# Optimization experiments

Measured on AMD Instinct MI355X. Metric: run time of the kernel, lower is better.

## Reference

```python
import jax, jax.numpy as jnp
import numpy as np

B, C, L, H = 4, 128, 4096, 4
GROUPS, EPS = 32, 1e-5


def group_norm(x, gamma, beta):
    # x: [B, C, L]; normalize per (batch, group) over (C//G, L)
    b, c, l = x.shape
    xg = x.reshape(b, GROUPS, c // GROUPS, l)
    mu = jnp.mean(xg, axis=(2, 3), keepdims=True)
    var = jnp.var(xg, axis=(2, 3), keepdims=True)
    xn = ((xg - mu) * jax.lax.rsqrt(var + EPS)).reshape(b, c, l)
    return xn * gamma[None, :, None] + beta[None, :, None]


def setup_inputs() -> dict:
    key = jax.random.key(0)
    k1, k2, k3 = jax.random.split(key, 3)
    return {
        "x": jax.random.normal(k1, (B, C, L), dtype=jnp.float32),
        "w_qkv": jax.random.normal(k2, (3 * C, C), dtype=jnp.float32) * 0.02,
        "w_proj": jax.random.normal(k3, (C, C), dtype=jnp.float32) * 0.02,
        "b_proj": jnp.zeros((C,), dtype=jnp.float32),
        "gn_gamma": jnp.ones((C,), dtype=jnp.float32),
        "gn_beta": jnp.zeros((C,), dtype=jnp.float32),
    }


def reference(x, w_qkv, w_proj, b_proj, gn_gamma, gn_beta):
    b, c, l = x.shape
    hd = c // H
    h = group_norm(x, gn_gamma, gn_beta)
    # 1x1 conv == channel matmul: [B, 3C, L]
    qkv = jnp.einsum('oc,bcl->bol', w_qkv, h)
    # torch reshape(B*H, 3C/H, L).chunk(3, dim=1): per-head contiguous slices
    qkv = qkv.reshape(b, H, 3 * hd, l)
    q, k, v = qkv[:, :, :hd], qkv[:, :, hd:2 * hd], qkv[:, :, 2 * hd:]
    scale = 1.0 / np.sqrt(np.sqrt(hd)).astype(np.float32)
    attn = jnp.einsum('bhct,bhcs->bhts', q * scale, k * scale)
    attn = jax.nn.softmax(attn, axis=-1)
    o = jnp.einsum('bhts,bhcs->bhct', attn, v).reshape(b, c, l)
    o = jnp.einsum('oc,bcl->bol', w_proj, o) + b_proj[None, :, None]
    return o + x
```

## Files before the change

### kernel.cpp

```cpp
#include <hip/hip_runtime.h>
#include <hip/hip_bf16.h>
#include <cstdint>
#include <cstddef>


#define B_ 4
#define C_ 128
#define L_ 4096
#define H_ 4
#define HD_ 32
#define NG_ 32
#define CPG_ 4
#define EPS_ 1e-5f
#define QKSCALE_ 0.5050097650430367f

typedef __attribute__((ext_vector_type(8))) short bf16x8;
typedef __attribute__((ext_vector_type(8))) unsigned short u16x8;
typedef __attribute__((ext_vector_type(4))) float f32x4;
typedef __attribute__((ext_vector_type(2))) _Float16 f16x2;
typedef __attribute__((ext_vector_type(4))) _Float16 f16x4;

#if __has_builtin(__builtin_amdgcn_exp2f)
#define EXP2F(x) __builtin_amdgcn_exp2f(x)
#else
#define EXP2F(x) exp2f(x)
#endif

#if __has_builtin(__builtin_amdgcn_mfma_f32_16x16x16f16)
#define MFMA_PV(a, b, c) __builtin_amdgcn_mfma_f32_16x16x16f16((a), (b), (c), 0, 0, 0)
#else
#define MFMA_PV(a, b, c) __builtin_amdgcn_mfma_f32_16x16x16f16((a), (b), (c), 0, 0, 0)
#endif

__device__ __forceinline__ float bu2f(unsigned short u) {
  return __builtin_bit_cast(float, (unsigned int)(((unsigned int)u) << 16));
}
__device__ __forceinline__ unsigned short f2bu(float f) {
  unsigned int u = __builtin_bit_cast(unsigned int, f);
  unsigned int r = (u + 0x7fffu + ((u >> 16) & 1u)) >> 16;
  return (unsigned short)r;
}
__device__ __forceinline__ float4 u42f4(ushort4 u) {
  return make_float4(bu2f(u.x), bu2f(u.y), bu2f(u.z), bu2f(u.w));
}
__device__ __forceinline__ unsigned int pkbf(float a, float b) {
  return (unsigned int)f2bu(a) | ((unsigned int)f2bu(b) << 16);
}
__device__ __forceinline__ f16x2 pkhf2(float a, float b) {
#if __has_builtin(__builtin_amdgcn_cvt_pkrtz)
  return __builtin_bit_cast(f16x2, __builtin_amdgcn_cvt_pkrtz(a, b));
#else
  f16x2 r;
  r[0] = (_Float16)a;
  r[1] = (_Float16)b;
  return r;
#endif
}
__device__ __forceinline__ unsigned int pkhf(float a, float b) {
  return __builtin_bit_cast(unsigned int, pkhf2(a, b));
}

__device__ __forceinline__ bool detect_fast(const ushort* x) {
  __shared__ int flag_s;
  int t = threadIdx.x;
  if (t < 64) {
    int e = (x[t] >> 7) & 0xFF;
    unsigned long long m = __ballot((e < 64) || (e > 192));
    if (t == 0) flag_s = (__popcll(m) > 4) ? 1 : 0;
  }
  __syncthreads();
  return flag_s != 0;
}

__device__ __forceinline__ float4 ldx4(const void* x, size_t idx, bool f32) {
  if (f32) return *((const float4*)x + (idx >> 2));
  ushort4 u = *((const ushort4*)x + (idx >> 2));
  return u42f4(u);
}

__global__ __launch_bounds__(256) void gn_stats(const void* __restrict__ x,
                                                const void* __restrict__ wq,
                                                const void* __restrict__ wp,
                                                const void* __restrict__ bp,
                                                const void* __restrict__ gm,
                                                const void* __restrict__ bt,
                                                ushort* __restrict__ wq_b,
                                                ushort* __restrict__ wp_b,
                                                float* __restrict__ bp_f,
                                                float2* __restrict__ gn_ab) {
  bool f32 = detect_fast((const ushort*)x);
  int blk = blockIdx.x;
  int t = threadIdx.x;

  if (blk >= 128) {
    int i0 = ((blk - 128) * 256 + t) * 8;
#pragma unroll
    for (int k = 0; k < 8; ++k) {
      int i = i0 + k;
      if (i >= 65664) break;
      if (i < 49152) {
        wq_b[i] = f32 ? f2bu(((const float*)wq)[i]) : ((const ushort*)wq)[i];
      } else if (i < 65536) {
        int off = i - 49152;
        wp_b[off] = f32 ? f2bu(((const float*)wp)[off]) : ((const ushort*)wp)[off];
      } else {
        int off = i - 65536;
        bp_f[off] = f32 ? ((const float*)bp)[off] : bu2f(((const ushort*)bp)[off]);
      }
    }
    return;
  }

  int b = blk >> 5, g = blk & 31;
  size_t base = ((size_t)b * C_ + (size_t)g * CPG_) * L_;

  float s = 0.f, ss = 0.f;
#pragma unroll
  for (int i = 0; i < 16; ++i) {
    size_t e = base + i * 1024 + t * 4;
    float4 f = ldx4(x, e, f32);
    s += f.x + f.y + f.z + f.w;
    ss += f.x * f.x + f.y * f.y + f.z * f.z + f.w * f.w;
  }
#pragma unroll
  for (int m = 32; m >= 1; m >>= 1) {
    s += __shfl_xor(s, m, 64);
    ss += __shfl_xor(ss, m, 64);
  }
  __shared__ float red[4][2];
  int wv = t >> 6;
  if ((t & 63) == 0) { red[wv][0] = s; red[wv][1] = ss; }
  __syncthreads();
  float ts = red[0][0] + red[1][0] + red[2][0] + red[3][0];
  float tss = red[0][1] + red[1][1] + red[2][1] + red[3][1];
  float mu = ts * (1.0f / 16384.0f);
  float var = tss * (1.0f / 16384.0f) - mu * mu;
  float rs = rsqrtf(var + EPS_);

  if (t < CPG_) {
    int gi = g * CPG_ + t;
    float ga = f32 ? ((const float*)gm)[gi] : bu2f(((const ushort*)gm)[gi]);
    float be = f32 ? ((const float*)bt)[gi] : bu2f(((const ushort*)bt)[gi]);
    gn_ab[b * C_ + gi] = make_float2(ga * rs, be - mu * ga * rs);
  }
}

__global__ __launch_bounds__(256) void qkv_kernel(const ushort* __restrict__ wq_b,
                                                  const void* __restrict__ x,
                                                  const float2* __restrict__ gn_ab,
                                                  ushort* __restrict__ Qt,
                                                  ushort* __restrict__ Kt,
                                                  ushort* __restrict__ Vb) {
  bool f32 = detect_fast((const ushort*)x);
  __shared__ alignas(16) ushort Hs[64][136];
  __shared__ alignas(16) float Ls[64][69];

  int lx = blockIdx.x, oz = blockIdx.y, b = blockIdx.z;
  int t = threadIdx.x;
  int w = t >> 6, lane = t & 63, l16 = lane & 15, q = lane >> 4, q8 = q * 8;

  {
    int u = t & 63, lh = (t >> 6) * 16;
    int c0 = 2 * u;
    float2 ab0 = gn_ab[b * C_ + c0];
    float2 ab1 = gn_ab[b * C_ + c0 + 1];
    size_t xo = ((size_t)b * C_ + c0) * L_ + (size_t)lx * 64 + lh;
#pragma unroll
    for (int j = 0; j < 4; ++j) {
      float4 f0 = ldx4(x, xo + j * 4, f32);
      float4 f1 = ldx4(x, xo + L_ + j * 4, f32);
      float n0[4] = {f0.x * ab0.x + ab0.y, f0.y * ab0.x + ab0.y,
                     f0.z * ab0.x + ab0.y, f0.w * ab0.x + ab0.y};
      float n1[4] = {f1.x * ab1.x + ab1.y, f1.y * ab1.x + ab1.y,
                     f1.z * ab1.x + ab1.y, f1.w * ab1.x + ab1.y};
#pragma unroll
      for (int k = 0; k < 4; ++k)
        *(unsigned int*)&Hs[lh + j * 4 + k][c0] = pkbf(n0[k], n1[k]);
    }
  }
  __syncthreads();

  for (int j = 0; j < 2; ++j) {
    int oy = oz * 2 + j;
    const ushort* wg = wq_b + (size_t)(oy * 64 + w * 16 + l16) * C_;

    f32x4 acc[4] = {{0.f, 0.f, 0.f, 0.f}, {0.f, 0.f, 0.f, 0.f},
                    {0.f, 0.f, 0.f, 0.f}, {0.f, 0.f, 0.f, 0.f}};
#pragma unroll
    for (int kc = 0; kc < 4; ++kc) {
      bf16x8 aw = *(const bf16x8*)(wg + kc * 32 + q8);
#pragma unroll
      for (int nb = 0; nb < 4; ++nb) {
        bf16x8 bh = *(const bf16x8*)&Hs[nb * 16 + l16][kc * 32 + q8];
        acc[nb] = __builtin_amdgcn_mfma_f32_16x16x32_bf16(aw, bh, acc[nb], 0, 0, 0);
      }
    }
    __syncthreads();
#pragma unroll
    for (int nb = 0; nb < 4; ++nb)
#pragma unroll
      for (int r = 0; r < 4; ++r)
        Ls[nb * 16 + l16][w * 16 + 4 * q + r] = acc[nb][r];
    __syncthreads();

#pragma unroll
    for (int hhalf = 0; hhalf < 2; ++hhalf) {
      int hh = oy * 2 + hhalf;
      int type = hh % 3, head = hh / 3;
      size_t bh = (size_t)b * H_ + head;
      if (type == 2) {
        int c_loc = t >> 3, l8 = (t & 7) * 8;
        float v[8];
#pragma unroll
        for (int jj = 0; jj < 8; ++jj) v[jj] = Ls[l8 + jj][hhalf * 32 + c_loc];
        uint4 u;
        u.x = pkhf(v[0], v[1]);
        u.y = pkhf(v[2], v[3]);
        u.z = pkhf(v[4], v[5]);
        u.w = pkhf(v[6], v[7]);
        *(uint4*)(Vb + (bh * 32 + c_loc) * L_ + (size_t)lx * 64 + l8) = u;
      } else {
        ushort* dst = type ? Kt : Qt;
        int l = t >> 2, seg = (t & 3) * 8;
        const float* src = &Ls[l][hhalf * 32 + seg];
        uint4 u;
        u.x = pkbf(src[0] * QKSCALE_, src[1] * QKSCALE_);
        u.y = pkbf(src[2] * QKSCALE_, src[3] * QKSCALE_);
        u.z = pkbf(src[4] * QKSCALE_, src[5] * QKSCALE_);
        u.w = pkbf(src[6] * QKSCALE_, src[7] * QKSCALE_);
        *(uint4*)(dst + ((bh * L_) + lx * 64 + l) * 32 + seg) = u;
      }
    }
  }
}

__global__ __launch_bounds__(256) void attn_kernel(const ushort* __restrict__ Qt,
                                                   const ushort* __restrict__ Kt,
                                                   const ushort* __restrict__ Vb,
                                                   ushort* __restrict__ ot) {
  __shared__ alignas(16) ushort Ks[2][4096];
  __shared__ alignas(16) ushort Vs[2][32][136];

  int t = threadIdx.x;
  int w = t >> 6, lane = t & 63, l16 = lane & 15, q = lane >> 4;
  int tq0 = blockIdx.x * 64;
  int bh = blockIdx.y;
  int b = bh >> 2, head = bh & 3;
  const ushort* Qg = Qt + ((size_t)bh * L_ + tq0) * 32;
  const ushort* Kg = Kt + (size_t)bh * L_ * 32;
  const ushort* Vg = Vb + (size_t)bh * 32 * L_;

  int krow = (t & 15) | ((t >> 6) << 4);
  int kq8 = ((t >> 4) & 3) * 8;
  const ushort* kgp = Kg + (size_t)krow * 32 + kq8;
  int vc = t >> 3, vsl = (t & 7) * 8;
  const ushort* vgp = Vg + (size_t)vc * L_ + vsl;
  int trow = w * 16 + l16;
  int q8 = q * 8, q4 = q * 4;

  bf16x8 qfrag = *(const bf16x8*)(Qg + (size_t)trow * 32 + q8);

  *(uint4*)&Ks[0][t * 8] = *(const uint4*)kgp;
  *(uint4*)&Ks[0][2048 + t * 8] = *(const uint4*)(kgp + 2048);
  *(uint4*)&Vs[0][vc][vsl] = *(const uint4*)vgp;
  *(uint4*)&Vs[0][vc][64 + vsl] = *(const uint4*)(vgp + 64);
  __syncthreads();

  f32x4 accA = {0.f, 0.f, 0.f, 0.f};
  f32x4 accB = {0.f, 0.f, 0.f, 0.f};
  float lpart = 0.f;
  const ushort* kg_n = kgp + 4096;
  const ushort* vg_n = vgp + 128;

#pragma unroll 2
  for (int it = 0; it < 32; ++it) {
    int bc = it & 1;
    if (it < 31) {
      *(uint4*)&Ks[bc ^ 1][t * 8] = *(const uint4*)kg_n;
      *(uint4*)&Ks[bc ^ 1][2048 + t * 8] = *(const uint4*)(kg_n + 2048);
      *(uint4*)&Vs[bc ^ 1][vc][vsl] = *(const uint4*)vg_n;
      *(uint4*)&Vs[bc ^ 1][vc][64 + vsl] = *(const uint4*)(vg_n + 64);
      kg_n += 4096;
      vg_n += 128;
    }

#pragma unroll
    for (int hh2 = 0; hh2 < 2; ++hh2) {
      const ushort* kf = &Ks[bc][hh2 * 2048 + lane * 8];
      f32x4 sf[4];
#pragma unroll
      for (int n = 0; n < 4; ++n) {
        bf16x8 ak = *(const bf16x8*)(kf + n * 512);
        f32x4 z = {0.f, 0.f, 0.f, 0.f};
        sf[n] = __builtin_amdgcn_mfma_f32_16x16x32_bf16(ak, qfrag, z, 0, 0, 0);
      }
#pragma unroll
      for (int n = 0; n < 4; ++n) {
        float p0 = EXP2F(sf[n][0]);
        float p1 = EXP2F(sf[n][1]);
        float p2 = EXP2F(sf[n][2]);
        float p3 = EXP2F(sf[n][3]);
        lpart += (p0 + p1) + (p2 + p3);
        f16x2 e01 = pkhf2(p0, p1);
        f16x2 e23 = pkhf2(p2, p3);
        f16x4 pb = __builtin_shufflevector(e01, e23, 0, 1, 2, 3);
        f16x4 va0 = *(const f16x4*)&Vs[bc][l16][hh2 * 64 + n * 16 + q4];
        f16x4 va1 = *(const f16x4*)&Vs[bc][16 + l16][hh2 * 64 + n * 16 + q4];
        accA = MFMA_PV(va0, pb, accA);
        accB = MFMA_PV(va1, pb, accB);
      }
    }
    __syncthreads();
  }

  lpart += __shfl_xor(lpart, 16, 64);
  lpart += __shfl_xor(lpart, 32, 64);
  float inv = 1.0f / lpart;

  __syncthreads();
  ushort* Ep = &Ks[0][0];
#pragma unroll
  for (int r = 0; r < 2; ++r) {
    *(unsigned int*)&Ep[trow * 40 + q4 + 2 * r] =
        pkbf(accA[2 * r] * inv, accA[2 * r + 1] * inv);
    *(unsigned int*)&Ep[trow * 40 + 16 + q4 + 2 * r] =
        pkbf(accB[2 * r] * inv, accB[2 * r + 1] * inv);
  }
  __syncthreads();
  {
    int row = t >> 2, seg = (t & 3) * 8;
    *(uint4*)(ot + ((size_t)b * L_ + tq0 + row) * C_ + head * 32 + seg) =
        *(const uint4*)&Ep[row * 40 + seg];
  }
}

__global__ __launch_bounds__(256) void proj_kernel(const ushort* __restrict__ wp_b,
                                                   const float* __restrict__ bias,
                                                   const void* __restrict__ x,
                                                   const ushort* __restrict__ ot,
                                                   void* __restrict__ out) {
  bool f32 = detect_fast((const ushort*)x);
  __shared__ alignas(16) float Ls[64][37];

  int lx = blockIdx.x, oy = blockIdx.y, b = blockIdx.z;
  int t = threadIdx.x;
  int w = t >> 6, lane = t & 63, l16 = lane & 15, q = lane >> 4, q8 = q * 8;

  const ushort* wg = wp_b + (size_t)(oy * 64 + w * 16 + l16) * C_;
  const ushort* og = ot + ((size_t)b * L_ + (size_t)lx * 32) * C_;

  f32x4 acc[2] = {{0.f, 0.f, 0.f, 0.f}, {0.f, 0.f, 0.f, 0.f}};
#pragma unroll
  for (int kc = 0; kc < 4; ++kc) {
    bf16x8 aw = *(const bf16x8*)(wg + kc * 32 + q8);
#pragma unroll
    for (int nb = 0; nb < 2; ++nb) {
      bf16x8 bo = *(const bf16x8*)(og + (size_t)(nb * 16 + l16) * C_ + kc * 32 + q8);
      acc[nb] = __builtin_amdgcn_mfma_f32_16x16x32_bf16(aw, bo, acc[nb], 0, 0, 0);
    }
  }
#pragma unroll
  for (int nb = 0; nb < 2; ++nb)
#pragma unroll
    for (int r = 0; r < 4; ++r)
      Ls[w * 16 + 4 * q + r][nb * 16 + l16] = acc[nb][r];
  __syncthreads();

  {
    int o_loc = t >> 2, ls0 = (t & 3) * 8;
    float bv = bias[oy * 64 + o_loc];
    size_t off = ((size_t)b * C_ + oy * 64 + o_loc) * L_ + (size_t)lx * 32 + ls0;
#pragma unroll
    for (int jj = 0; jj < 2; ++jj) {
      float4 xf = ldx4(x, off + jj * 4, f32);
      const float* sp = &Ls[o_loc][ls0 + jj * 4];
      float4 r = make_float4(sp[0] + bv + xf.x, sp[1] + bv + xf.y,
                             sp[2] + bv + xf.z, sp[3] + bv + xf.w);
      if (f32) {
        *(float4*)((float*)out + off + jj * 4) = r;
      } else {
        *(ushort4*)((ushort*)out + off + jj * 4) =
            make_ushort4(f2bu(r.x), f2bu(r.y), f2bu(r.z), f2bu(r.w));
      }
    }
  }
}

extern "C" void kernel_launch(void* const* d_in, const int* in_sizes, int n_in,
                              void* d_out, int out_size, void* d_ws, size_t ws_size,
                              hipStream_t stream) {
  const void* x      = d_in[0];
  const void* w_qkv  = d_in[1];
  const void* w_proj = d_in[2];
  const void* b_proj = d_in[3];
  const void* gamma  = d_in[4];
  const void* beta   = d_in[5];

  char* wsb = (char*)d_ws;
  ushort* wq_b  = (ushort*)(wsb + 0);
  ushort* wp_b  = (ushort*)(wsb + 98304);
  float*  bp_f  = (float*)(wsb + 131072);
  float2* gn_ab = (float2*)(wsb + 131584);
  ushort* Qt    = (ushort*)(wsb + 8388608);
  ushort* Kt    = (ushort*)(wsb + 12582912);
  ushort* Vb    = (ushort*)(wsb + 16777216);
  ushort* ot    = (ushort*)(wsb + 20971520);

  gn_stats<<<dim3(161), dim3(256), 0, stream>>>(x, w_qkv, w_proj, b_proj, gamma, beta,
                                                wq_b, wp_b, bp_f, gn_ab);
  qkv_kernel<<<dim3(L_ / 64, 3, B_), dim3(256), 0, stream>>>(wq_b, x, gn_ab, Qt, Kt, Vb);
  attn_kernel<<<dim3(L_ / 64, B_ * H_), dim3(256), 0, stream>>>(Qt, Kt, Vb, ot);
  proj_kernel<<<dim3(L_ / 32, C_ / 64, B_), dim3(256), 0, stream>>>(wp_b, bp_f, x, ot, d_out);
}
```

Baseline: 152.5 us.

## Process 128 queries per attention block and compute row sums via MFMA

Each attention block now handles two 64-query tiles, so every K/V tile staged in shared memory is reused twice, and the grid is halved. The softmax denominator is now accumulated with an extra MFMA against a ones vector instead of scalar adds plus cross-lane shuffles. This cuts global and LDS traffic per query and removes VALU reduction work, at the cost of more registers per thread and half as many blocks (512) to spread over the CUs.

```diff
diff --git a/kernel.cpp b/kernel.cpp
--- a/kernel.cpp
+++ b/kernel.cpp
@@ -26,11 +26,7 @@
 #define EXP2F(x) exp2f(x)
 #endif
 
-#if __has_builtin(__builtin_amdgcn_mfma_f32_16x16x16f16)
 #define MFMA_PV(a, b, c) __builtin_amdgcn_mfma_f32_16x16x16f16((a), (b), (c), 0, 0, 0)
-#else
-#define MFMA_PV(a, b, c) __builtin_amdgcn_mfma_f32_16x16x16f16((a), (b), (c), 0, 0, 0)
-#endif
 
 __device__ __forceinline__ float bu2f(unsigned short u) {
   return __builtin_bit_cast(float, (unsigned int)(((unsigned int)u) << 16));
@@ -243,7 +239,7 @@
 
   int t = threadIdx.x;
   int w = t >> 6, lane = t & 63, l16 = lane & 15, q = lane >> 4;
-  int tq0 = blockIdx.x * 64;
+  int tq0 = blockIdx.x * 128;
   int bh = blockIdx.y;
   int b = bh >> 2, head = bh & 3;
   const ushort* Qg = Qt + ((size_t)bh * L_ + tq0) * 32;
@@ -258,7 +254,11 @@
   int trow = w * 16 + l16;
   int q8 = q * 8, q4 = q * 4;
 
-  bf16x8 qfrag = *(const bf16x8*)(Qg + (size_t)trow * 32 + q8);
+  bf16x8 qfrag0 = *(const bf16x8*)(Qg + (size_t)trow * 32 + q8);
+  bf16x8 qfrag1 = *(const bf16x8*)(Qg + (size_t)(64 + trow) * 32 + q8);
+  f16x4 ones;
+#pragma unroll
+  for (int i = 0; i < 4; ++i) ones[i] = (_Float16)1.0f;
 
   *(uint4*)&Ks[0][t * 8] = *(const uint4*)kgp;
   *(uint4*)&Ks[0][2048 + t * 8] = *(const uint4*)(kgp + 2048);
@@ -266,9 +266,9 @@
   *(uint4*)&Vs[0][vc][64 + vsl] = *(const uint4*)(vgp + 64);
   __syncthreads();
 
-  f32x4 accA = {0.f, 0.f, 0.f, 0.f};
-  f32x4 accB = {0.f, 0.f, 0.f, 0.f};
-  float lpart = 0.f;
+  f32x4 aA0 = {0.f, 0.f, 0.f, 0.f}, aB0 = {0.f, 0.f, 0.f, 0.f};
+  f32x4 aA1 = {0.f, 0.f, 0.f, 0.f}, aB1 = {0.f, 0.f, 0.f, 0.f};
+  f32x4 aL0 = {0.f, 0.f, 0.f, 0.f}, aL1 = {0.f, 0.f, 0.f, 0.f};
   const ushort* kg_n = kgp + 4096;
   const ushort* vg_n = vgp + 128;
 
@@ -287,50 +287,78 @@
 #pragma unroll
     for (int hh2 = 0; hh2 < 2; ++hh2) {
       const ushort* kf = &Ks[bc][hh2 * 2048 + lane * 8];
-      f32x4 sf[4];
+      bf16x8 ak0 = *(const bf16x8*)(kf);
+      bf16x8 ak1 = *(const bf16x8*)(kf + 512);
+      bf16x8 ak2 = *(const bf16x8*)(kf + 1024);
+      bf16x8 ak3 = *(const bf16x8*)(kf + 1536);
+      f32x4 z = {0.f, 0.f, 0.f, 0.f};
+      f32x4 sf0[4], sf1[4];
+      sf0[0] = __builtin_amdgcn_mfma_f32_16x16x32_bf16(ak0, qfrag0, z, 0, 0, 0);
+      sf0[1] = __builtin_amdgcn_mfma_f32_16x16x32_bf16(ak1, qfrag0, z, 0, 0, 0);
+      sf0[2] = __builtin_amdgcn_mfma_f32_16x16x32_bf16(ak2, qfrag0, z, 0, 0, 0);
+      sf0[3] = __builtin_amdgcn_mfma_f32_16x16x32_bf16(ak3, qfrag0, z, 0, 0, 0);
+      sf1[0] = __builtin_amdgcn_mfma_f32_16x16x32_bf16(ak0, qfrag1, z, 0, 0, 0);
+      sf1[1] = __builtin_amdgcn_mfma_f32_16x16x32_bf16(ak1, qfrag1, z, 0, 0, 0);
+      sf1[2] = __builtin_amdgcn_mfma_f32_16x16x32_bf16(ak2, qfrag1, z, 0, 0, 0);
+      sf1[3] = __builtin_amdgcn_mfma_f32_16x16x32_bf16(ak3, qfrag1, z, 0, 0, 0);
+
 #pragma unroll
       for (int n = 0; n < 4; ++n) {
-        bf16x8 ak = *(const bf16x8*)(kf + n * 512);
-        f32x4 z = {0.f, 0.f, 0.f, 0.f};
-        sf[n] = __builtin_amdgcn_mfma_f32_16x16x32_bf16(ak, qfrag, z, 0, 0, 0);
-      }
-#pragma unroll
-      for (int n = 0; n < 4; ++n) {
-        float p0 = EXP2F(sf[n][0]);
-        float p1 = EXP2F(sf[n][1]);
-        float p2 = EXP2F(sf[n][2]);
-        float p3 = EXP2F(sf[n][3]);
-        lpart += (p0 + p1) + (p2 + p3);
-        f16x2 e01 = pkhf2(p0, p1);
-        f16x2 e23 = pkhf2(p2, p3);
-        f16x4 pb = __builtin_shufflevector(e01, e23, 0, 1, 2, 3);
         f16x4 va0 = *(const f16x4*)&Vs[bc][l16][hh2 * 64 + n * 16 + q4];
         f16x4 va1 = *(const f16x4*)&Vs[bc][16 + l16][hh2 * 64 + n * 16 + q4];
-        accA = MFMA_PV(va0, pb, accA);
-        accB = MFMA_PV(va1, pb, accB);
+        {
+          float p0 = EXP2F(sf0[n][0]);
+          float p1 = EXP2F(sf0[n][1]);
+          float p2 = EXP2F(sf0[n][2]);
+          float p3 = EXP2F(sf0[n][3]);
+          f16x2 e01 = pkhf2(p0, p1);
+          f16x2 e23 = pkhf2(p2, p3);
+          f16x4 pb = __builtin_shufflevector(e01, e23, 0, 1, 2, 3);
+          aA0 = MFMA_PV(va0, pb, aA0);
+          aB0 = MFMA_PV(va1, pb, aB0);
+          aL0 = MFMA_PV(ones, pb, aL0);
+        }
+        {
+          float p0 = EXP2F(sf1[n][0]);
+          float p1 = EXP2F(sf1[n][1]);
+          float p2 = EXP2F(sf1[n][2]);
+          float p3 = EXP2F(sf1[n][3]);
+          f16x2 e01 = pkhf2(p0, p1);
+          f16x2 e23 = pkhf2(p2, p3);
+          f16x4 pb = __builtin_shufflevector(e01, e23, 0, 1, 2, 3);
+          aA1 = MFMA_PV(va0, pb, aA1);
+          aB1 = MFMA_PV(va1, pb, aB1);
+          aL1 = MFMA_PV(ones, pb, aL1);
+        }
       }
     }
     __syncthreads();
   }
 
-  lpart += __shfl_xor(lpart, 16, 64);
-  lpart += __shfl_xor(lpart, 32, 64);
-  float inv = 1.0f / lpart;
+  float inv0 = 1.0f / aL0[0];
+  float inv1 = 1.0f / aL1[0];
 
   __syncthreads();
   ushort* Ep = &Ks[0][0];
 #pragma unroll
   for (int r = 0; r < 2; ++r) {
     *(unsigned int*)&Ep[trow * 40 + q4 + 2 * r] =
-        pkbf(accA[2 * r] * inv, accA[2 * r + 1] * inv);
+        pkbf(aA0[2 * r] * inv0, aA0[2 * r + 1] * inv0);
     *(unsigned int*)&Ep[trow * 40 + 16 + q4 + 2 * r] =
-        pkbf(accB[2 * r] * inv, accB[2 * r + 1] * inv);
+        pkbf(aB0[2 * r] * inv0, aB0[2 * r + 1] * inv0);
+    *(unsigned int*)&Ep[(64 + trow) * 40 + q4 + 2 * r] =
+        pkbf(aA1[2 * r] * inv1, aA1[2 * r + 1] * inv1);
+    *(unsigned int*)&Ep[(64 + trow) * 40 + 16 + q4 + 2 * r] =
+        pkbf(aB1[2 * r] * inv1, aB1[2 * r + 1] * inv1);
   }
   __syncthreads();
   {
     int row = t >> 2, seg = (t & 3) * 8;
-    *(uint4*)(ot + ((size_t)b * L_ + tq0 + row) * C_ + head * 32 + seg) =
-        *(const uint4*)&Ep[row * 40 + seg];
+#pragma unroll
+    for (int p = 0; p < 2; ++p) {
+      *(uint4*)(ot + ((size_t)b * L_ + tq0 + p * 64 + row) * C_ + head * 32 + seg) =
+          *(const uint4*)&Ep[(p * 64 + row) * 40 + seg];
+    }
   }
 }
 
@@ -409,6 +437,6 @@
   gn_stats<<<dim3(161), dim3(256), 0, stream>>>(x, w_qkv, w_proj, b_proj, gamma, beta,
                                                 wq_b, wp_b, bp_f, gn_ab);
   qkv_kernel<<<dim3(L_ / 64, 3, B_), dim3(256), 0, stream>>>(wq_b, x, gn_ab, Qt, Kt, Vb);
-  attn_kernel<<<dim3(L_ / 64, B_ * H_), dim3(256), 0, stream>>>(Qt, Kt, Vb, ot);
+  attn_kernel<<<dim3(L_ / 128, B_ * H_), dim3(256), 0, stream>>>(Qt, Kt, Vb, ot);
   proj_kernel<<<dim3(L_ / 32, C_ / 64, B_), dim3(256), 0, stream>>>(wp_b, bp_f, x, ot, d_out);
 }
```

Measured after the change: 149.4 us. 1.02x faster.
